# Performance work log

Measured on AMD Instinct MI355X. Metric: run time of the kernel, lower is better.

The kernel has to match this reference:

```python
import jax, jax.numpy as jnp
import numpy as np

D = 32        # bond_dim == virtual_dim
EPS = 1e-5    # BatchNorm eps


def unfold(x, dim, size):
    """torch.Tensor.unfold(dim, size, step=size): split dim into (n, size), window dim goes last."""
    n = x.shape[dim] // size
    new_shape = x.shape[:dim] + (n, size) + x.shape[dim + 1:]
    return jnp.moveaxis(x.reshape(new_shape), dim + 1, -1)


def mps_level(x, cores, label):
    """Batched MPS contraction over P independent patch modules.
    x: (b, C, S, P) site values; cores: (P, S, 2C, D, D); label: (P, O, D, D).
    Feature map phi = [x, 1-x] along channel dim (feature_dim = 2C).
    Returns (b, O, P)."""
    phi = jnp.concatenate([x, 1.0 - x], axis=1)               # (b, 2C, S, P)
    mats = jnp.einsum('bfsp,psfij->bpsij', phi, cores)        # (b, P, S, D, D)
    M = mats[:, :, 0]
    for s in range(1, mats.shape[2]):                          # S=4 fixed, unrolled
        M = jnp.matmul(M, mats[:, :, s])
    # boundary vectors e0 on both sides of the label core
    out = jnp.einsum('bpj,poj->bpo', M[:, :, 0, :], label[:, :, :, 0])
    return out.transpose(0, 2, 1)                              # (b, O, P)


def mps_final(x, cores, label):
    """Single MPS over S sites. x: (b, C, S); cores: (S, 2C, D, D); label: (O, D, D)."""
    phi = jnp.concatenate([x, 1.0 - x], axis=1)               # (b, 2C, S)
    mats = jnp.einsum('bfs,sfij->bsij', phi, cores)           # (b, S, D, D)
    v0 = mats[:, 0, 0, :]                                      # e0 @ mat_0 -> (b, D)
    def step(v, m):
        return jnp.einsum('bi,bij->bj', v, m), None
    v, _ = jax.lax.scan(step, v0, jnp.moveaxis(mats[:, 1:], 1, 0))
    return jnp.einsum('bj,oj->bo', v, label[:, :, 0])          # (b, O)


def batchnorm1d(y, gamma, beta):
    """BatchNorm1d on (b, C, L): per-channel stats over (b, L), training mode."""
    mean = y.mean(axis=(0, 2), keepdims=True)
    var = y.var(axis=(0, 2), keepdims=True)
    return (y - mean) / jnp.sqrt(var + EPS) * gamma[None, :, None] + beta[None, :, None]


def setup_inputs() -> dict:
    key = jax.random.key(0)
    ks = jax.random.split(key, 16)
    eye = jnp.eye(D, dtype=jnp.float32)
    std = 0.01  # near-identity init (torchmps-style), bumped from 1e-9 for numerics
    x = jax.random.uniform(ks[0], (64, 3, 128, 128), dtype=jnp.float32)
    # level 1: 256 modules, 4 sites, feature_dim = 2*48 = 96
    cores1 = eye + std * jax.random.normal(ks[1], (256, 4, 96, D, D), dtype=jnp.float32)
    label1 = std * jax.random.normal(ks[2], (256, D, D, D), dtype=jnp.float32)
    g1 = jnp.ones((D,), jnp.float32); b1 = jnp.zeros((D,), jnp.float32)
    # level 2: 64 modules, feature_dim = 2*D = 64
    cores2 = eye + std * jax.random.normal(ks[3], (64, 4, 2 * D, D, D), dtype=jnp.float32)
    label2 = std * jax.random.normal(ks[4], (64, D, D, D), dtype=jnp.float32)
    g2 = jnp.ones((D,), jnp.float32); b2 = jnp.zeros((D,), jnp.float32)
    # level 3: 16 modules
    cores3 = eye + std * jax.random.normal(ks[5], (16, 4, 2 * D, D, D), dtype=jnp.float32)
    label3 = std * jax.random.normal(ks[6], (16, D, D, D), dtype=jnp.float32)
    g3 = jnp.ones((D,), jnp.float32); b3 = jnp.zeros((D,), jnp.float32)
    # final MPS: 16 sites, feature_dim = 2*D, output_dim = 1
    coresF = eye + std * jax.random.normal(ks[7], (16, 2 * D, D, D), dtype=jnp.float32)
    labelF = std * jax.random.normal(ks[8], (1, D, D), dtype=jnp.float32)
    return {"x": x, "cores1": cores1, "label1": label1, "g1": g1, "b1": b1,
            "cores2": cores2, "label2": label2, "g2": g2, "b2": b2,
            "cores3": cores3, "label3": label3, "g3": g3, "b3": b3,
            "coresF": coresF, "labelF": labelF}


def reference(x, cores1, label1, g1, b1, cores2, label2, g2, b2,
              cores3, label3, g3, b3, coresF, labelF):
    b = x.shape[0]
    # kScale unfold: (b,3,128,128) -> (b,32,32,48)  (raw torch reshape reinterpretation)
    x = unfold(x, 2, 32); x = unfold(x, 3, 32)
    x = x.reshape(b, 32, 32, -1)
    # level-1 patching: -> (b, 48, 4, 256)
    x = unfold(x, 2, 16); x = unfold(x, 3, 16)
    x = x.reshape(b, 48, 4, -1)
    y = batchnorm1d(mps_level(x, cores1, label1), g1, b1)      # (b, D, 256)
    y = y.reshape(b, D, 16, 16)
    y = unfold(y, 2, 8); y = unfold(y, 3, 8)
    y = y.reshape(b, D, 4, -1)                                 # (b, D, 4, 64)
    y = batchnorm1d(mps_level(y, cores2, label2), g2, b2)      # (b, D, 64)
    y = y.reshape(b, D, 8, 8)
    y = unfold(y, 2, 4); y = unfold(y, 3, 4)
    y = y.reshape(b, D, 4, -1)                                 # (b, D, 4, 16)
    y = batchnorm1d(mps_level(y, cores3, label3), g3, b3)      # (b, D, 16)
    y = mps_final(y, coresF, labelF)                           # (b, 1)
    return y.reshape(b)
```

## Files before the change

kernel.cpp:

```cpp
#include <hip/hip_runtime.h>

typedef unsigned int u32;
typedef unsigned short u16;
typedef float f32x4 __attribute__((ext_vector_type(4)));
typedef u32 u32x4 __attribute__((ext_vector_type(4)));
typedef short s16x8 __attribute__((ext_vector_type(8)));

__device__ __forceinline__ u32 f2bf(float f) {
  u32 x = __builtin_bit_cast(u32, f);
  return (x + 0x7FFFu + ((x >> 16) & 1u)) >> 16;
}
__device__ __forceinline__ float bfu2f(u16 u) {
  u32 x = ((u32)u) << 16;
  return __builtin_bit_cast(float, x);
}
__device__ __forceinline__ u32 cvtpk(float lo, float hi) {
  u32 r;
  asm("v_cvt_pk_bf16_f32 %0, %1, %2" : "=v"(r) : "v"(lo), "v"(hi));
  return r;
}
__device__ __forceinline__ u32x4 mk8(const float* v) {
  u32x4 u;
  u.x = cvtpk(v[0], v[1]); u.y = cvtpk(v[2], v[3]);
  u.z = cvtpk(v[4], v[5]); u.w = cvtpk(v[6], v[7]);
  return u;
}
__device__ __forceinline__ void mfma16(f32x4& acc, u32x4 a, u32x4 b) {
  acc = __builtin_amdgcn_mfma_f32_16x16x32_bf16(
      __builtin_bit_cast(s16x8, a), __builtin_bit_cast(s16x8, b), acc, 0, 0, 0);
}

__global__ __launch_bounds__(256) void k_gather1(const float* __restrict__ x,
                                                 float* __restrict__ phi1) {
  __shared__ float tile[64][65];
  const int t = threadIdx.x;
  const int base = blockIdx.x * 64;
  const int lb = t & 63;
  {
    const int flat = base + lb;
    const int c = flat >> 14;
    const int r1 = flat & 16383;
    const int h1 = r1 >> 12;
    const int r2 = r1 & 4095;
    const int w1 = r2 >> 10;
    const int r3 = r2 & 1023;
    const int h2 = r3 >> 5;
    const int w2 = r3 & 31;
    const int xoff = c * 16384 + h1 * 4096 + h2 * 128 + w1 * 32 + w2;
    for (int b = t >> 6; b < 64; b += 4)
      tile[lb][b] = x[b * 49152 + xoff];
  }
  __syncthreads();
  for (int q = t >> 6; q < 64; q += 4) {
    const int flat = base + q;
    const int a = flat / 1536;
    const int rem = flat % 1536;
    const int e = rem / 48, gg = rem % 48;
    const int e1 = e >> 4, e2 = e & 15, g1 = gg >> 4, g2 = gg & 15;
    const int tt = a * 6 + e1 * 3 + g1;
    const int F = tt >> 2, Sx = tt & 3, Pp = e2 * 16 + g2;
    const float val = tile[q][lb];
    const int idx = ((Pp * 4 + Sx) * 96 + F) * 64 + lb;
    phi1[idx] = val;
    phi1[idx + 3072] = 1.0f - val;
  }
}

__global__ __launch_bounds__(512) void k_level1(const float* __restrict__ phi1,
                                                const float* __restrict__ cores1,
                                                const float* __restrict__ label1,
                                                float* __restrict__ y1raw) {
  __shared__ float phi_s[96 * 64];
  __shared__ float v_s[64 * 33];
  __shared__ float red_s[8 * 4 * 16 * 17];
  __shared__ float lab_s[1024];
  const int p = blockIdx.x, t = threadIdx.x;
  const int w = t >> 6, lane = t & 63, g = lane >> 4, l15 = lane & 15;
  const int jm = w & 1, fq = w >> 1;
  const float* phip = phi1 + p * 24576;
  const float* Cp = cores1 + p * 393216;

  {
    const float4* s4 = (const float4*)phip;
    float4* d4 = (float4*)phi_s;
#pragma unroll
    for (int k = 0; k < 3; ++k) d4[t + k * 512] = s4[t + k * 512];
  }
  __syncthreads();
  {
    const int rowj = jm * 16 + l15, colb = fq * 16 + l15;
    f32x4 acc = {0.f, 0.f, 0.f, 0.f};
    const float* A0 = Cp + rowj;
#pragma unroll
    for (int ks = 0; ks < 3; ++ks) {
      float av[8], bv[8];
#pragma unroll
      for (int e = 0; e < 8; ++e) {
        const int f = ks * 32 + g * 8 + e;
        av[e] = A0[f * 1024];
        bv[e] = phi_s[f * 64 + colb];
      }
      mfma16(acc, mk8(av), mk8(bv));
    }
#pragma unroll
    for (int r = 0; r < 4; ++r) v_s[colb * 33 + jm * 16 + g * 4 + r] = acc[r];
  }
  for (int s = 1; s < 4; ++s) {
    __syncthreads();
    float v8[4][8];
#pragma unroll
    for (int n = 0; n < 4; ++n)
#pragma unroll
      for (int e = 0; e < 8; ++e)
        v8[n][e] = v_s[(n * 16 + l15) * 33 + g * 8 + e];
    {
      const float4* s4 = (const float4*)(phip + s * 6144);
      float4* d4 = (float4*)phi_s;
#pragma unroll
      for (int k = 0; k < 3; ++k) d4[t + k * 512] = s4[t + k * 512];
    }
    const float* As = Cp + s * 98304 + fq * 24576 + g * 256 + jm * 16 + l15;
    float pf[6][8];
#pragma unroll
    for (int fi = 0; fi < 6; ++fi)
#pragma unroll
      for (int e = 0; e < 8; ++e) pf[fi][e] = As[fi * 1024 + e * 32];
    __syncthreads();
    f32x4 acc[4];
#pragma unroll
    for (int n = 0; n < 4; ++n) acc[n] = (f32x4){0.f, 0.f, 0.f, 0.f};
#pragma unroll
    for (int fo = 0; fo < 4; ++fo) {
#pragma unroll
      for (int fi = 0; fi < 6; ++fi) {
        const int f = fo * 6 + fi;
        const u32x4 afr = mk8(pf[fi]);
        if (f + 6 < 24) {
#pragma unroll
          for (int e = 0; e < 8; ++e) pf[fi][e] = As[(f + 6) * 1024 + e * 32];
        }
#pragma unroll
        for (int n = 0; n < 4; ++n) {
          const float phf = phi_s[(fq * 24 + f) * 64 + n * 16 + l15];
          float bv[8];
#pragma unroll
          for (int e = 0; e < 8; ++e) bv[e] = phf * v8[n][e];
          mfma16(acc[n], afr, mk8(bv));
        }
      }
    }
#pragma unroll
    for (int n = 0; n < 4; ++n)
#pragma unroll
      for (int r = 0; r < 4; ++r)
        red_s[((w * 4 + n) * 16 + g * 4 + r) * 17 + l15] = acc[n][r];
    __syncthreads();
    for (int i = t; i < 2048; i += 512) {
      const int b = i >> 5, j = i & 31;
      const int n = b >> 4, lb = b & 15, jj = j >> 4, row = j & 15;
      v_s[b * 33 + j] = red_s[(((jj)*4 + n) * 16 + row) * 17 + lb]
                      + red_s[(((jj + 2) * 4 + n) * 16 + row) * 17 + lb]
                      + red_s[(((jj + 4) * 4 + n) * 16 + row) * 17 + lb]
                      + red_s[(((jj + 6) * 4 + n) * 16 + row) * 17 + lb];
    }
  }
  __syncthreads();
  for (int i = t; i < 1024; i += 512)
    lab_s[(i & 31) * 32 + (i >> 5)] = label1[(p * 1024 + i) * 32];
  __syncthreads();
  {
    const int b = t & 63, og = t >> 6;
    float a[4] = {0.f, 0.f, 0.f, 0.f};
    for (int j = 0; j < 32; ++j) {
      const float vj = v_s[b * 33 + j];
#pragma unroll
      for (int r = 0; r < 4; ++r) a[r] += vj * lab_s[j * 32 + og * 4 + r];
    }
#pragma unroll
    for (int r = 0; r < 4; ++r)
      y1raw[((og * 4 + r) * 256 + p) * 64 + b] = a[r];
  }
}

__global__ __launch_bounds__(256) void k_bnpart(const float* __restrict__ y,
                                                float* __restrict__ part,
                                                int N) {
  __shared__ float rs[256], rq[256];
  const int o = blockIdx.x >> 3, c = blockIdx.x & 7;
  const int CH = N >> 3;
  const float* src = y + o * N + c * CH;
  const int t = threadIdx.x;
  float s = 0.f, q = 0.f;
  for (int i = t; i < CH; i += 256) { const float v = src[i]; s += v; q += v * v; }
  rs[t] = s; rq[t] = q;
  __syncthreads();
  for (int k = 128; k > 0; k >>= 1) {
    if (t < k) { rs[t] += rs[t + k]; rq[t] += rq[t + k]; }
    __syncthreads();
  }
  if (t == 0) {
    part[(o * 8 + c) * 2] = rs[0];
    part[(o * 8 + c) * 2 + 1] = rq[0];
  }
}

template <int LEVEL>
__global__ __launch_bounds__(512) void k_build(const float* __restrict__ yraw,
                                               const float* __restrict__ cores,
                                               u16* __restrict__ mats,
                                               float* __restrict__ v0,
                                               const float* __restrict__ part,
                                               const float* __restrict__ gamma,
                                               const float* __restrict__ beta) {
  constexpr int S = (LEVEL == 0) ? 16 : 4;
  constexpr int NQ = (LEVEL == 2) ? 2 : ((LEVEL == 3) ? 4 : 16);
  constexpr int NC = 1024 / NQ;
  constexpr int NTW = NC / 32;
  constexpr float BN_N = (LEVEL == 2) ? 16384.f : ((LEVEL == 3) ? 4096.f : 1024.f);
  __shared__ float phi_s[64 * 64];
  __shared__ float scsh_s[64];
  const int bid = blockIdx.x;
  const int p = bid / (S * NQ);
  const int rs = bid % (S * NQ);
  const int s = rs / NQ, nq = rs % NQ;
  if (s == 0 && nq != 0) return;
  const int t = threadIdx.x;
  const int w = t >> 6, lane = t & 63;
  const int g = lane >> 4, l15 = lane & 15;
  if (t < 32) {
    float sm = 0.f, sq = 0.f;
#pragma unroll
    for (int c = 0; c < 8; ++c) {
      sm += part[(t * 8 + c) * 2];
      sq += part[(t * 8 + c) * 2 + 1];
    }
    const float mean = sm / BN_N;
    const float var = sq / BN_N - mean * mean;
    const float sc = gamma[t] * rsqrtf(fmaxf(var, 0.f) + 1e-5f);
    scsh_s[2 * t] = sc;
    scsh_s[2 * t + 1] = beta[t] - mean * sc;
  }
  __syncthreads();
  for (int i = t; i < 2048; i += 512) {
    const int f = i >> 6, b = i & 63;
    int src;
    if (LEVEL == 2) {
      const int u = (s >> 1) * 8 + (p >> 3), vv = (s & 1) * 8 + (p & 7);
      src = (f * 256 + u * 16 + vv) * 64 + b;
    } else if (LEVEL == 3) {
      const int u = (s >> 1) * 4 + (p >> 2), vv = (s & 1) * 4 + (p & 3);
      src = (f * 64 + u * 8 + vv) * 64 + b;
    } else {
      src = (f * 16 + s) * 64 + b;
    }
    const float val = fmaf(yraw[src], scsh_s[2 * f], scsh_s[2 * f + 1]);
    phi_s[f * 64 + b] = val;
    phi_s[(f + 32) * 64 + b] = 1.0f - val;
  }
  __syncthreads();
  const float* Cb = cores + (p * S + s) * 65536;
  const int m = w & 3, nh = w >> 2;
  const int rowb = m * 16 + l15;
  float av[8];
#pragma unroll
  for (int e = 0; e < 8; ++e) av[e] = phi_s[(g * 8 + e) * 64 + rowb];
  const u32x4 afr0 = mk8(av);
#pragma unroll
  for (int e = 0; e < 8; ++e) av[e] = phi_s[(32 + g * 8 + e) * 64 + rowb];
  const u32x4 afr1 = mk8(av);
  if (s == 0) {
    const int col = nh * 16 + l15;
    f32x4 acc = {0.f, 0.f, 0.f, 0.f};
    float bv[8];
#pragma unroll
    for (int e = 0; e < 8; ++e) bv[e] = Cb[(g * 8 + e) * 1024 + col];
    mfma16(acc, afr0, mk8(bv));
#pragma unroll
    for (int e = 0; e < 8; ++e) bv[e] = Cb[(32 + g * 8 + e) * 1024 + col];
    mfma16(acc, afr1, mk8(bv));
#pragma unroll
    for (int r = 0; r < 4; ++r)
      v0[(p * 64 + m * 16 + g * 4 + r) * 32 + col] = acc[r];
  } else {
#pragma unroll 4
    for (int nt = 0; nt < NTW; ++nt) {
      const int col = nq * NC + (nh * NTW + nt) * 16 + l15;
      f32x4 acc = {0.f, 0.f, 0.f, 0.f};
      float bv[8];
#pragma unroll
      for (int e = 0; e < 8; ++e) bv[e] = Cb[(g * 8 + e) * 1024 + col];
      mfma16(acc, afr0, mk8(bv));
#pragma unroll
      for (int e = 0; e < 8; ++e) bv[e] = Cb[(32 + g * 8 + e) * 1024 + col];
      mfma16(acc, afr1, mk8(bv));
      u16* mp = mats + (((size_t)p * (S - 1) + (s - 1)) * 64 + m * 16 + g * 4) * 1024 + col;
#pragma unroll
      for (int r = 0; r < 4; ++r) mp[r * 1024] = (u16)f2bf(acc[r]);
    }
  }
}

template <int LEVEL>
__global__ __launch_bounds__(256) void k_chain(const float* __restrict__ v0,
                                               const u16* __restrict__ mats,
                                               const float* __restrict__ label,
                                               float* __restrict__ yraw) {
  constexpr int P = (LEVEL == 2) ? 64 : 16;
  constexpr int NB = (LEVEL == 2) ? 4 : 1;
  __shared__ float lab_s[1024];
  const int t = threadIdx.x, w = t >> 6, lane = t & 63;
  int p, b0;
  if (LEVEL == 2) { p = blockIdx.x >> 2; b0 = (blockIdx.x & 3) * 16 + w * 4; }
  else            { p = blockIdx.x >> 4; b0 = (blockIdx.x & 15) * 4 + w; }
  for (int i = t; i < 1024; i += 256)
    lab_s[(i & 31) * 32 + (i >> 5)] = label[(p * 1024 + i) * 32];
  __syncthreads();
  const int j = lane & 31;
#pragma unroll
  for (int bi = 0; bi < NB; ++bi) {
    const int b = b0 + bi;
    float v = v0[(p * 64 + b) * 32 + j];
#pragma unroll
    for (int s1 = 0; s1 < 3; ++s1) {
      const u16* M = mats + (((size_t)p * 3 + s1) * 64 + b) * 1024;
      float acc = 0.f;
#pragma unroll
      for (int i = 0; i < 32; ++i)
        acc += __shfl(v, i, 64) * bfu2f(M[i * 32 + j]);
      v = acc;
    }
    float out = 0.f;
#pragma unroll
    for (int jj = 0; jj < 32; ++jj)
      out += __shfl(v, jj, 64) * lab_s[jj * 32 + j];
    if (lane < 32) yraw[(j * P + p) * 64 + b] = out;
  }
}

__global__ __launch_bounds__(64) void k_chainF(const float* __restrict__ v0,
                                               const u16* __restrict__ mats,
                                               const float* __restrict__ labelF,
                                               float* __restrict__ out) {
  __shared__ u16 m_s[15 * 1024];
  const int lane = threadIdx.x, b = blockIdx.x, j = lane & 31;
  {
    uint4* dst = (uint4*)m_s;
#pragma unroll
    for (int s1 = 0; s1 < 15; ++s1) {
      const uint4* src = (const uint4*)(mats + ((size_t)s1 * 64 + b) * 1024);
      dst[s1 * 128 + lane] = src[lane];
      dst[s1 * 128 + 64 + lane] = src[64 + lane];
    }
  }
  float v = v0[b * 32 + j];
  __syncthreads();
  for (int s1 = 0; s1 < 15; ++s1) {
    float acc = 0.f;
#pragma unroll
    for (int i = 0; i < 32; ++i)
      acc += __shfl(v, i, 64) * bfu2f(m_s[s1 * 1024 + i * 32 + j]);
    v = acc;
  }
  float r = v * labelF[j * 32];
#pragma unroll
  for (int off = 16; off > 0; off >>= 1) r += __shfl_xor(r, off, 64);
  if (lane == 0) out[b] = r;
}

extern "C" void kernel_launch(void* const* d_in, const int* in_sizes, int n_in,
                              void* d_out, int out_size, void* d_ws, size_t ws_size,
                              hipStream_t stream) {
  (void)in_sizes; (void)n_in; (void)out_size; (void)ws_size;
  const float* x      = (const float*)d_in[0];
  const float* cores1 = (const float*)d_in[1];
  const float* label1 = (const float*)d_in[2];
  const float* g1     = (const float*)d_in[3];
  const float* b1     = (const float*)d_in[4];
  const float* cores2 = (const float*)d_in[5];
  const float* label2 = (const float*)d_in[6];
  const float* g2     = (const float*)d_in[7];
  const float* b2     = (const float*)d_in[8];
  const float* cores3 = (const float*)d_in[9];
  const float* label3 = (const float*)d_in[10];
  const float* g3     = (const float*)d_in[11];
  const float* b3     = (const float*)d_in[12];
  const float* coresF = (const float*)d_in[13];
  const float* labelF = (const float*)d_in[14];

  char* wsb = (char*)d_ws;
  size_t off = 0;
  auto alloc = [&](size_t bytes) -> char* {
    char* r = wsb + off;
    off += (bytes + 255) & ~(size_t)255;
    return r;
  };
  char* region0 = alloc(6291456ull * 4);
  float* phi1  = (float*)region0;
  u16*   mats2 = (u16*)region0;
  float* y1raw = (float*)alloc(524288ull * 4);
  float* v02   = (float*)alloc(131072ull * 4);
  float* y2raw = (float*)alloc(131072ull * 4);
  float* v03   = (float*)alloc(32768ull * 4);
  u16*   mats3 = (u16*)  alloc(3145728ull * 2);
  float* y3raw = (float*)alloc(32768ull * 4);
  float* v0F   = (float*)alloc(2048ull * 4);
  u16*   matsF = (u16*)  alloc(983040ull * 2);
  float* part1 = (float*)alloc(512 * 4);
  float* part2 = (float*)alloc(512 * 4);
  float* part3 = (float*)alloc(512 * 4);

  k_gather1<<<768, 256, 0, stream>>>(x, phi1);
  k_level1<<<256, 512, 0, stream>>>(phi1, cores1, label1, y1raw);
  k_bnpart<<<256, 256, 0, stream>>>(y1raw, part1, 16384);
  k_build<2><<<512, 512, 0, stream>>>(y1raw, cores2, mats2, v02, part1, g1, b1);
  k_chain<2><<<256, 256, 0, stream>>>(v02, mats2, label2, y2raw);
  k_bnpart<<<256, 256, 0, stream>>>(y2raw, part2, 4096);
  k_build<3><<<256, 512, 0, stream>>>(y2raw, cores3, mats3, v03, part2, g2, b2);
  k_chain<3><<<256, 256, 0, stream>>>(v03, mats3, label3, y3raw);
  k_bnpart<<<256, 256, 0, stream>>>(y3raw, part3, 1024);
  k_build<0><<<256, 512, 0, stream>>>(y3raw, coresF, matsF, v0F, part3, g3, b3);
  k_chainF<<<64, 64, 0, stream>>>(v0F, matsF, labelF, (float*)d_out);
}
```

Measured before the change: 181.3 us.

## Fuse BatchNorm partial statistics into producer kernels, drop k_bnpart launches

Removes the three standalone k_bnpart kernels. The level-1 and chain kernels now compute per-block sums and sums of squares of their outputs with wave shuffles or shared memory and write them to enlarged partial buffers. Each k_build kernel then reduces 256 partials per channel before computing the scale and shift. This saves three launches and one re-read of each activation tensor, at the cost of extra reduction work that is repeated in every build block.

```diff
diff --git a/kernel.cpp b/kernel.cpp
--- a/kernel.cpp
+++ b/kernel.cpp
@@ -69,7 +69,8 @@
 __global__ __launch_bounds__(512) void k_level1(const float* __restrict__ phi1,
                                                 const float* __restrict__ cores1,
                                                 const float* __restrict__ label1,
-                                                float* __restrict__ y1raw) {
+                                                float* __restrict__ y1raw,
+                                                float* __restrict__ part1) {
   __shared__ float phi_s[96 * 64];
   __shared__ float v_s[64 * 33];
   __shared__ float red_s[8 * 4 * 16 * 17];
@@ -179,28 +180,19 @@
 #pragma unroll
     for (int r = 0; r < 4; ++r)
       y1raw[((og * 4 + r) * 256 + p) * 64 + b] = a[r];
-  }
-}
-
-__global__ __launch_bounds__(256) void k_bnpart(const float* __restrict__ y,
-                                                float* __restrict__ part,
-                                                int N) {
-  __shared__ float rs[256], rq[256];
-  const int o = blockIdx.x >> 3, c = blockIdx.x & 7;
-  const int CH = N >> 3;
-  const float* src = y + o * N + c * CH;
-  const int t = threadIdx.x;
-  float s = 0.f, q = 0.f;
-  for (int i = t; i < CH; i += 256) { const float v = src[i]; s += v; q += v * v; }
-  rs[t] = s; rq[t] = q;
-  __syncthreads();
-  for (int k = 128; k > 0; k >>= 1) {
-    if (t < k) { rs[t] += rs[t + k]; rq[t] += rq[t + k]; }
-    __syncthreads();
-  }
-  if (t == 0) {
-    part[(o * 8 + c) * 2] = rs[0];
-    part[(o * 8 + c) * 2 + 1] = rq[0];
+#pragma unroll
+    for (int r = 0; r < 4; ++r) {
+      float sr = a[r], qr = a[r] * a[r];
+#pragma unroll
+      for (int off = 32; off > 0; off >>= 1) {
+        sr += __shfl_xor(sr, off, 64);
+        qr += __shfl_xor(qr, off, 64);
+      }
+      if (lane == 0) {
+        part1[p * 64 + (og * 4 + r) * 2] = sr;
+        part1[p * 64 + (og * 4 + r) * 2 + 1] = qr;
+      }
+    }
   }
 }
 
@@ -219,6 +211,7 @@
   constexpr float BN_N = (LEVEL == 2) ? 16384.f : ((LEVEL == 3) ? 4096.f : 1024.f);
   __shared__ float phi_s[64 * 64];
   __shared__ float scsh_s[64];
+  __shared__ float redp[32][8][2];
   const int bid = blockIdx.x;
   const int p = bid / (S * NQ);
   const int rs = bid % (S * NQ);
@@ -227,13 +220,22 @@
   const int t = threadIdx.x;
   const int w = t >> 6, lane = t & 63;
   const int g = lane >> 4, l15 = lane & 15;
+  if (t < 256) {
+    const int o = t >> 3, c = t & 7;
+    float sm = 0.f, sq = 0.f;
+    for (int k = 0; k < 32; ++k) {
+      const int ch = c * 32 + k;
+      sm += part[ch * 64 + o * 2];
+      sq += part[ch * 64 + o * 2 + 1];
+    }
+    redp[o][c][0] = sm;
+    redp[o][c][1] = sq;
+  }
+  __syncthreads();
   if (t < 32) {
     float sm = 0.f, sq = 0.f;
 #pragma unroll
-    for (int c = 0; c < 8; ++c) {
-      sm += part[(t * 8 + c) * 2];
-      sq += part[(t * 8 + c) * 2 + 1];
-    }
+    for (int c = 0; c < 8; ++c) { sm += redp[t][c][0]; sq += redp[t][c][1]; }
     const float mean = sm / BN_N;
     const float var = sq / BN_N - mean * mean;
     const float sc = gamma[t] * rsqrtf(fmaxf(var, 0.f) + 1e-5f);
@@ -304,10 +306,12 @@
 __global__ __launch_bounds__(256) void k_chain(const float* __restrict__ v0,
                                                const u16* __restrict__ mats,
                                                const float* __restrict__ label,
-                                               float* __restrict__ yraw) {
+                                               float* __restrict__ yraw,
+                                               float* __restrict__ partN) {
   constexpr int P = (LEVEL == 2) ? 64 : 16;
   constexpr int NB = (LEVEL == 2) ? 4 : 1;
   __shared__ float lab_s[1024];
+  __shared__ float bnp_s[4][2][32];
   const int t = threadIdx.x, w = t >> 6, lane = t & 63;
   int p, b0;
   if (LEVEL == 2) { p = blockIdx.x >> 2; b0 = (blockIdx.x & 3) * 16 + w * 4; }
@@ -316,6 +320,7 @@
     lab_s[(i & 31) * 32 + (i >> 5)] = label[(p * 1024 + i) * 32];
   __syncthreads();
   const int j = lane & 31;
+  float cs = 0.f, cq = 0.f;
 #pragma unroll
   for (int bi = 0; bi < NB; ++bi) {
     const int b = b0 + bi;
@@ -333,7 +338,18 @@
 #pragma unroll
     for (int jj = 0; jj < 32; ++jj)
       out += __shfl(v, jj, 64) * lab_s[jj * 32 + j];
-    if (lane < 32) yraw[(j * P + p) * 64 + b] = out;
+    if (lane < 32) {
+      yraw[(j * P + p) * 64 + b] = out;
+      cs += out;
+      cq += out * out;
+    }
+  }
+  if (lane < 32) { bnp_s[w][0][j] = cs; bnp_s[w][1][j] = cq; }
+  __syncthreads();
+  if (t < 64) {
+    const int jj = t & 31, h = t >> 5;
+    partN[blockIdx.x * 64 + jj * 2 + h] =
+        bnp_s[0][h][jj] + bnp_s[1][h][jj] + bnp_s[2][h][jj] + bnp_s[3][h][jj];
   }
 }
 
@@ -405,19 +421,16 @@
   float* y3raw = (float*)alloc(32768ull * 4);
   float* v0F   = (float*)alloc(2048ull * 4);
   u16*   matsF = (u16*)  alloc(983040ull * 2);
-  float* part1 = (float*)alloc(512 * 4);
-  float* part2 = (float*)alloc(512 * 4);
-  float* part3 = (float*)alloc(512 * 4);
+  float* part1 = (float*)alloc(16384ull * 4);
+  float* part2 = (float*)alloc(16384ull * 4);
+  float* part3 = (float*)alloc(16384ull * 4);
 
   k_gather1<<<768, 256, 0, stream>>>(x, phi1);
-  k_level1<<<256, 512, 0, stream>>>(phi1, cores1, label1, y1raw);
-  k_bnpart<<<256, 256, 0, stream>>>(y1raw, part1, 16384);
+  k_level1<<<256, 512, 0, stream>>>(phi1, cores1, label1, y1raw, part1);
   k_build<2><<<512, 512, 0, stream>>>(y1raw, cores2, mats2, v02, part1, g1, b1);
-  k_chain<2><<<256, 256, 0, stream>>>(v02, mats2, label2, y2raw);
-  k_bnpart<<<256, 256, 0, stream>>>(y2raw, part2, 4096);
+  k_chain<2><<<256, 256, 0, stream>>>(v02, mats2, label2, y2raw, part2);
   k_build<3><<<256, 512, 0, stream>>>(y2raw, cores3, mats3, v03, part2, g2, b2);
-  k_chain<3><<<256, 256, 0, stream>>>(v03, mats3, label3, y3raw);
-  k_bnpart<<<256, 256, 0, stream>>>(y3raw, part3, 1024);
+  k_chain<3><<<256, 256, 0, stream>>>(v03, mats3, label3, y3raw, part3);
   k_build<0><<<256, 512, 0, stream>>>(y3raw, coresF, matsF, v0F, part3, g3, b3);
   k_chainF<<<64, 64, 0, stream>>>(v0F, matsF, labelF, (float*)d_out);
 }
```

Result: slower. 230.1 us (+26.9%).

## Fuse tail stages into one cooperative persistent kernel with grid syncs

Applied to the files above, without the earlier changes.

Replaces the seven launches after level-2 build (chain2, bnpart, build3, chain3, bnpart, buildF, chainF) with a single cooperative kernel of 256 blocks × 512 threads that runs each stage in turn, separated by grid.sync. The aim is to remove per-launch overhead and launch gaps on these small, latency-bound stages. In exchange it adds grid-wide barrier costs, leaves some blocks idle in certain phases, and changes the work split, for example the level-2 chain now uses 2 batches per wave instead of 4.

```diff
diff --git a/kernel.cpp b/kernel.cpp
--- a/kernel.cpp
+++ b/kernel.cpp
@@ -1,4 +1,7 @@
 #include <hip/hip_runtime.h>
+#include <hip/hip_cooperative_groups.h>
+
+namespace cg = cooperative_groups;
 
 typedef unsigned int u32;
 typedef unsigned short u16;
@@ -300,71 +303,244 @@
   }
 }
 
+__device__ __forceinline__ void bnpart_body(char* smem, const float* y,
+                                            float* part, int N, int t) {
+  float* rs = (float*)smem;
+  float* rq = rs + 512;
+  const int o = blockIdx.x >> 3, c = blockIdx.x & 7;
+  const int CH = N >> 3;
+  const float* src = y + o * N + c * CH;
+  float s = 0.f, q = 0.f;
+  for (int i = t; i < CH; i += 512) { const float v = src[i]; s += v; q += v * v; }
+  rs[t] = s; rq[t] = q;
+  __syncthreads();
+  for (int k = 256; k > 0; k >>= 1) {
+    if (t < k) { rs[t] += rs[t + k]; rq[t] += rq[t + k]; }
+    __syncthreads();
+  }
+  if (t == 0) {
+    part[(o * 8 + c) * 2] = rs[0];
+    part[(o * 8 + c) * 2 + 1] = rq[0];
+  }
+  __syncthreads();
+}
+
 template <int LEVEL>
-__global__ __launch_bounds__(256) void k_chain(const float* __restrict__ v0,
-                                               const u16* __restrict__ mats,
-                                               const float* __restrict__ label,
-                                               float* __restrict__ yraw) {
-  constexpr int P = (LEVEL == 2) ? 64 : 16;
-  constexpr int NB = (LEVEL == 2) ? 4 : 1;
-  __shared__ float lab_s[1024];
-  const int t = threadIdx.x, w = t >> 6, lane = t & 63;
-  int p, b0;
-  if (LEVEL == 2) { p = blockIdx.x >> 2; b0 = (blockIdx.x & 3) * 16 + w * 4; }
-  else            { p = blockIdx.x >> 4; b0 = (blockIdx.x & 15) * 4 + w; }
-  for (int i = t; i < 1024; i += 256)
-    lab_s[(i & 31) * 32 + (i >> 5)] = label[(p * 1024 + i) * 32];
-  __syncthreads();
-  const int j = lane & 31;
-#pragma unroll
-  for (int bi = 0; bi < NB; ++bi) {
-    const int b = b0 + bi;
-    float v = v0[(p * 64 + b) * 32 + j];
-#pragma unroll
-    for (int s1 = 0; s1 < 3; ++s1) {
-      const u16* M = mats + (((size_t)p * 3 + s1) * 64 + b) * 1024;
-      float acc = 0.f;
-#pragma unroll
-      for (int i = 0; i < 32; ++i)
-        acc += __shfl(v, i, 64) * bfu2f(M[i * 32 + j]);
-      v = acc;
-    }
-    float out = 0.f;
-#pragma unroll
-    for (int jj = 0; jj < 32; ++jj)
-      out += __shfl(v, jj, 64) * lab_s[jj * 32 + j];
-    if (lane < 32) yraw[(j * P + p) * 64 + b] = out;
-  }
-}
-
-__global__ __launch_bounds__(64) void k_chainF(const float* __restrict__ v0,
-                                               const u16* __restrict__ mats,
-                                               const float* __restrict__ labelF,
-                                               float* __restrict__ out) {
-  __shared__ u16 m_s[15 * 1024];
-  const int lane = threadIdx.x, b = blockIdx.x, j = lane & 31;
+__device__ __forceinline__ void build_body(char* smem, const float* yraw,
+                                           const float* cores, u16* mats,
+                                           float* v0, const float* part,
+                                           const float* gamma, const float* beta,
+                                           int t) {
+  constexpr int S = (LEVEL == 0) ? 16 : 4;
+  constexpr int NQ = (LEVEL == 3) ? 4 : 16;
+  constexpr int NC = 1024 / NQ;
+  constexpr int NTW = NC / 32;
+  constexpr float BN_N = (LEVEL == 3) ? 4096.f : 1024.f;
+  float* phi_s = (float*)smem;
+  float* scsh_s = (float*)(smem + 16384);
+  const int bid = blockIdx.x;
+  const int p = bid / (S * NQ);
+  const int rsd = bid % (S * NQ);
+  const int s = rsd / NQ, nq = rsd % NQ;
+  const bool active = !(s == 0 && nq != 0);
+  if (active) {
+    const int w = t >> 6, lane = t & 63;
+    const int g = lane >> 4, l15 = lane & 15;
+    if (t < 32) {
+      float sm = 0.f, sq = 0.f;
+#pragma unroll
+      for (int c = 0; c < 8; ++c) {
+        sm += part[(t * 8 + c) * 2];
+        sq += part[(t * 8 + c) * 2 + 1];
+      }
+      const float mean = sm / BN_N;
+      const float var = sq / BN_N - mean * mean;
+      const float sc = gamma[t] * rsqrtf(fmaxf(var, 0.f) + 1e-5f);
+      scsh_s[2 * t] = sc;
+      scsh_s[2 * t + 1] = beta[t] - mean * sc;
+    }
+    __syncthreads();
+    for (int i = t; i < 2048; i += 512) {
+      const int f = i >> 6, b = i & 63;
+      int src;
+      if (LEVEL == 3) {
+        const int u = (s >> 1) * 4 + (p >> 2), vv = (s & 1) * 4 + (p & 3);
+        src = (f * 64 + u * 8 + vv) * 64 + b;
+      } else {
+        src = (f * 16 + s) * 64 + b;
+      }
+      const float val = fmaf(yraw[src], scsh_s[2 * f], scsh_s[2 * f + 1]);
+      phi_s[f * 64 + b] = val;
+      phi_s[(f + 32) * 64 + b] = 1.0f - val;
+    }
+    __syncthreads();
+    const float* Cb = cores + (p * S + s) * 65536;
+    const int m = w & 3, nh = w >> 2;
+    const int rowb = m * 16 + l15;
+    float av[8];
+#pragma unroll
+    for (int e = 0; e < 8; ++e) av[e] = phi_s[(g * 8 + e) * 64 + rowb];
+    const u32x4 afr0 = mk8(av);
+#pragma unroll
+    for (int e = 0; e < 8; ++e) av[e] = phi_s[(32 + g * 8 + e) * 64 + rowb];
+    const u32x4 afr1 = mk8(av);
+    if (s == 0) {
+      const int col = nh * 16 + l15;
+      f32x4 acc = {0.f, 0.f, 0.f, 0.f};
+      float bv[8];
+#pragma unroll
+      for (int e = 0; e < 8; ++e) bv[e] = Cb[(g * 8 + e) * 1024 + col];
+      mfma16(acc, afr0, mk8(bv));
+#pragma unroll
+      for (int e = 0; e < 8; ++e) bv[e] = Cb[(32 + g * 8 + e) * 1024 + col];
+      mfma16(acc, afr1, mk8(bv));
+#pragma unroll
+      for (int r = 0; r < 4; ++r)
+        v0[(p * 64 + m * 16 + g * 4 + r) * 32 + col] = acc[r];
+    } else {
+#pragma unroll 4
+      for (int nt = 0; nt < NTW; ++nt) {
+        const int col = nq * NC + (nh * NTW + nt) * 16 + l15;
+        f32x4 acc = {0.f, 0.f, 0.f, 0.f};
+        float bv[8];
+#pragma unroll
+        for (int e = 0; e < 8; ++e) bv[e] = Cb[(g * 8 + e) * 1024 + col];
+        mfma16(acc, afr0, mk8(bv));
+#pragma unroll
+        for (int e = 0; e < 8; ++e) bv[e] = Cb[(32 + g * 8 + e) * 1024 + col];
+        mfma16(acc, afr1, mk8(bv));
+        u16* mp = mats + (((size_t)p * (S - 1) + (s - 1)) * 64 + m * 16 + g * 4) * 1024 + col;
+#pragma unroll
+        for (int r = 0; r < 4; ++r) mp[r * 1024] = (u16)f2bf(acc[r]);
+      }
+    }
+    __syncthreads();
+  }
+}
+
+__global__ __launch_bounds__(512) void k_tail(
+    const float* __restrict__ v02, const u16* __restrict__ mats2,
+    const float* __restrict__ label2, float* __restrict__ y2raw,
+    float* __restrict__ part2,
+    const float* __restrict__ cores3, u16* __restrict__ mats3,
+    float* __restrict__ v03, const float* __restrict__ g2,
+    const float* __restrict__ b2,
+    const float* __restrict__ label3, float* __restrict__ y3raw,
+    float* __restrict__ part3,
+    const float* __restrict__ coresF, u16* __restrict__ matsF,
+    float* __restrict__ v0F, const float* __restrict__ g3,
+    const float* __restrict__ b3,
+    const float* __restrict__ labelF, float* __restrict__ outp) {
+  __shared__ __align__(16) char smem[30720];
+  cg::grid_group grid = cg::this_grid();
+  const int t = threadIdx.x;
+
   {
-    uint4* dst = (uint4*)m_s;
-#pragma unroll
-    for (int s1 = 0; s1 < 15; ++s1) {
-      const uint4* src = (const uint4*)(mats + ((size_t)s1 * 64 + b) * 1024);
-      dst[s1 * 128 + lane] = src[lane];
-      dst[s1 * 128 + 64 + lane] = src[64 + lane];
-    }
-  }
-  float v = v0[b * 32 + j];
-  __syncthreads();
-  for (int s1 = 0; s1 < 15; ++s1) {
-    float acc = 0.f;
-#pragma unroll
-    for (int i = 0; i < 32; ++i)
-      acc += __shfl(v, i, 64) * bfu2f(m_s[s1 * 1024 + i * 32 + j]);
-    v = acc;
-  }
-  float r = v * labelF[j * 32];
-#pragma unroll
-  for (int off = 16; off > 0; off >>= 1) r += __shfl_xor(r, off, 64);
-  if (lane == 0) out[b] = r;
+    float* lab_s = (float*)smem;
+    const int bid = blockIdx.x;
+    const int p = bid >> 2;
+    const int w = t >> 6, lane = t & 63, j = lane & 31;
+    for (int i = t; i < 1024; i += 512)
+      lab_s[(i & 31) * 32 + (i >> 5)] = label2[(p * 1024 + i) * 32];
+    __syncthreads();
+    const int b0 = (bid & 3) * 16 + w * 2;
+#pragma unroll
+    for (int bi = 0; bi < 2; ++bi) {
+      const int b = b0 + bi;
+      float v = v02[(p * 64 + b) * 32 + j];
+#pragma unroll
+      for (int s1 = 0; s1 < 3; ++s1) {
+        const u16* M = mats2 + (((size_t)p * 3 + s1) * 64 + b) * 1024;
+        float acc = 0.f;
+#pragma unroll
+        for (int i = 0; i < 32; ++i)
+          acc += __shfl(v, i, 64) * bfu2f(M[i * 32 + j]);
+        v = acc;
+      }
+      float o2 = 0.f;
+#pragma unroll
+      for (int jj = 0; jj < 32; ++jj)
+        o2 += __shfl(v, jj, 64) * lab_s[jj * 32 + j];
+      if (lane < 32) y2raw[(j * 64 + p) * 64 + b] = o2;
+    }
+    __syncthreads();
+  }
+  __threadfence();
+  grid.sync();
+
+  bnpart_body(smem, y2raw, part2, 4096, t);
+  __threadfence();
+  grid.sync();
+
+  build_body<3>(smem, y2raw, cores3, mats3, v03, part2, g2, b2, t);
+  __threadfence();
+  grid.sync();
+
+  {
+    float* lab_s = (float*)smem;
+    const int p = blockIdx.x >> 4;
+    const int w = t >> 6, lane = t & 63, j = lane & 31;
+    for (int i = t; i < 1024; i += 512)
+      lab_s[(i & 31) * 32 + (i >> 5)] = label3[(p * 1024 + i) * 32];
+    __syncthreads();
+    if (w < 4) {
+      const int b = (blockIdx.x & 15) * 4 + w;
+      float v = v03[(p * 64 + b) * 32 + j];
+#pragma unroll
+      for (int s1 = 0; s1 < 3; ++s1) {
+        const u16* M = mats3 + (((size_t)p * 3 + s1) * 64 + b) * 1024;
+        float acc = 0.f;
+#pragma unroll
+        for (int i = 0; i < 32; ++i)
+          acc += __shfl(v, i, 64) * bfu2f(M[i * 32 + j]);
+        v = acc;
+      }
+      float o3 = 0.f;
+#pragma unroll
+      for (int jj = 0; jj < 32; ++jj)
+        o3 += __shfl(v, jj, 64) * lab_s[jj * 32 + j];
+      if (lane < 32) y3raw[(j * 16 + p) * 64 + b] = o3;
+    }
+    __syncthreads();
+  }
+  __threadfence();
+  grid.sync();
+
+  bnpart_body(smem, y3raw, part3, 1024, t);
+  __threadfence();
+  grid.sync();
+
+  build_body<0>(smem, y3raw, coresF, matsF, v0F, part3, g3, b3, t);
+  __threadfence();
+  grid.sync();
+
+  if (blockIdx.x < 64) {
+    u16* m_s = (u16*)smem;
+    const int b = blockIdx.x;
+    {
+      uint4* dst = (uint4*)m_s;
+      for (int i = t; i < 1920; i += 512) {
+        const int s1 = i >> 7, k = i & 127;
+        dst[i] = ((const uint4*)(matsF + ((size_t)s1 * 64 + b) * 1024))[k];
+      }
+    }
+    __syncthreads();
+    if (t < 64) {
+      const int lane = t, j = lane & 31;
+      float v = v0F[b * 32 + j];
+      for (int s1 = 0; s1 < 15; ++s1) {
+        float acc = 0.f;
+#pragma unroll
+        for (int i = 0; i < 32; ++i)
+          acc += __shfl(v, i, 64) * bfu2f(m_s[s1 * 1024 + i * 32 + j]);
+        v = acc;
+      }
+      float r = v * labelF[j * 32];
+#pragma unroll
+      for (int off = 16; off > 0; off >>= 1) r += __shfl_xor(r, off, 64);
+      if (lane == 0) outp[b] = r;
+    }
+  }
 }
 
 extern "C" void kernel_launch(void* const* d_in, const int* in_sizes, int n_in,
@@ -408,16 +584,21 @@
   float* part1 = (float*)alloc(512 * 4);
   float* part2 = (float*)alloc(512 * 4);
   float* part3 = (float*)alloc(512 * 4);
+  float* outp  = (float*)d_out;
 
   k_gather1<<<768, 256, 0, stream>>>(x, phi1);
   k_level1<<<256, 512, 0, stream>>>(phi1, cores1, label1, y1raw);
   k_bnpart<<<256, 256, 0, stream>>>(y1raw, part1, 16384);
   k_build<2><<<512, 512, 0, stream>>>(y1raw, cores2, mats2, v02, part1, g1, b1);
-  k_chain<2><<<256, 256, 0, stream>>>(v02, mats2, label2, y2raw);
-  k_bnpart<<<256, 256, 0, stream>>>(y2raw, part2, 4096);
-  k_build<3><<<256, 512, 0, stream>>>(y2raw, cores3, mats3, v03, part2, g2, b2);
-  k_chain<3><<<256, 256, 0, stream>>>(v03, mats3, label3, y3raw);
-  k_bnpart<<<256, 256, 0, stream>>>(y3raw, part3, 1024);
-  k_build<0><<<256, 512, 0, stream>>>(y3raw, coresF, matsF, v0F, part3, g3, b3);
-  k_chainF<<<64, 64, 0, stream>>>(v0F, matsF, labelF, (float*)d_out);
-}
+
+  const u16* mats2c = mats2;
+  void* args[] = {
+    (void*)&v02,    (void*)&mats2c, (void*)&label2, (void*)&y2raw, (void*)&part2,
+    (void*)&cores3, (void*)&mats3,  (void*)&v03,    (void*)&g2,    (void*)&b2,
+    (void*)&label3, (void*)&y3raw,  (void*)&part3,
+    (void*)&coresF, (void*)&matsF,  (void*)&v0F,    (void*)&g3,    (void*)&b3,
+    (void*)&labelF, (void*)&outp
+  };
+  hipLaunchCooperativeKernel((const void*)k_tail, dim3(256), dim3(512),
+                             args, 0, stream);
+}
```

After: 595.1 us. +228.2%, slower.
